# Performance work log

Hardware: AMD Instinct MI355X
Metric: run time of the kernel (lower is better)

Reference implementation:

```python
import jax, jax.numpy as jnp
import numpy as np

T, N, E, F, H, LH = 24, 50000, 1_600_000, 16, 64, 128


def setup_inputs() -> dict:
    key = jax.random.key(0)
    ks = jax.random.split(key, 16)
    s = 0.1  # small init scale
    return {
        "x_seq": jax.random.normal(ks[0], (T, N, F), jnp.float32),
        "edge_index": jax.random.randint(ks[1], (2, E), 0, N, dtype=jnp.int32),
        "W1": jax.random.normal(ks[2], (F, H), jnp.float32) * s,
        "b1": jax.random.normal(ks[3], (H,), jnp.float32) * s,
        "W2": jax.random.normal(ks[4], (H, H), jnp.float32) * s,
        "b2": jax.random.normal(ks[5], (H,), jnp.float32) * s,
        "W_ih": jax.random.normal(ks[6], (4 * LH, H), jnp.float32) * s,
        "W_hh": jax.random.normal(ks[7], (4 * LH, LH), jnp.float32) * s,
        "b_ih": jax.random.normal(ks[8], (4 * LH,), jnp.float32) * s,
        "b_hh": jax.random.normal(ks[9], (4 * LH,), jnp.float32) * s,
        "Wf1": jax.random.normal(ks[10], (LH, 32), jnp.float32) * s,
        "bf1": jax.random.normal(ks[11], (32,), jnp.float32) * s,
        "Wf2": jax.random.normal(ks[12], (32, 1), jnp.float32) * s,
        "bf2": jax.random.normal(ks[13], (1,), jnp.float32) * s,
    }


def reference(x_seq, edge_index, W1, b1, W2, b2, W_ih, W_hh, b_ih, b_hh, Wf1, bf1, Wf2, bf2):
    Nn = x_seq.shape[1]
    lh = W_hh.shape[1]
    src, dst = edge_index[0], edge_index[1]

    # GCN symmetric norm with self-loops: deg counts incoming edges + self-loop
    deg = jax.ops.segment_sum(jnp.ones(src.shape[0], x_seq.dtype), dst, num_segments=Nn) + 1.0
    dinv = jax.lax.rsqrt(deg)
    enorm = dinv[src] * dinv[dst]          # (E,)
    snorm = dinv * dinv                    # (N,) self-loop norm

    def agg(xw):  # xw: (N, H')  -> D^-1/2 (A+I) D^-1/2 xw
        out = jax.ops.segment_sum(xw[src] * enorm[:, None], dst, num_segments=Nn)
        return out + xw * snorm[:, None]

    def gcn_step(_, x_t):  # x_t: (N, F)
        h = jax.nn.relu(agg(x_t @ W1) + b1)
        h = jax.nn.relu(agg(h @ W2) + b2)
        return None, h

    _, h_seq = jax.lax.scan(gcn_step, None, x_seq)  # (T, N, H)

    # single-layer LSTM (torch gate order i, f, g, o); only final h needed
    def lstm_step(carry, x_t):
        h, c = carry
        g = x_t @ W_ih.T + b_ih + h @ W_hh.T + b_hh
        i, f, gg, o = jnp.split(g, 4, axis=-1)
        c = jax.nn.sigmoid(f) * c + jax.nn.sigmoid(i) * jnp.tanh(gg)
        h = jax.nn.sigmoid(o) * jnp.tanh(c)
        return (h, c), None

    h0 = jnp.zeros((Nn, lh), x_seq.dtype)
    (hT, _), _ = jax.lax.scan(lstm_step, (h0, h0), h_seq)

    z = jax.nn.relu(hT @ Wf1 + bf1)
    return (z @ Wf2 + bf2)[:, 0]  # (N,)
```

## Files before the change

### kernel.cpp

```cpp
#include <hip/hip_runtime.h>
#include <hip/hip_bf16.h>
#include <math.h>


typedef short s16x8 __attribute__((ext_vector_type(8)));
typedef float f32x16 __attribute__((ext_vector_type(16)));
typedef unsigned long long u64;
union AF { s16x8 v; u64 q[2]; };

__device__ __forceinline__ float sigf(float x) { return 1.f / (1.f + __expf(-x)); }
__device__ __forceinline__ float tanhfast(float x) { return 1.f - 2.f / (1.f + __expf(2.f * x)); }

__device__ __forceinline__ unsigned bfr(float x) {
    union { float f; unsigned u; } c; c.f = x;
    return (c.u + 0x7fffu + ((c.u >> 16) & 1u)) >> 16;
}
__device__ __forceinline__ void bsplit(float x, unsigned short& hi, unsigned short& lo) {
    unsigned h = bfr(x);
    union { unsigned u; float f; } hf; hf.u = h << 16;
    hi = (unsigned short)h;
    lo = (unsigned short)bfr(x - hf.f);
}
__device__ __forceinline__ float bf2f(unsigned short b) {
    union { unsigned u; float f; } c; c.u = ((unsigned)b) << 16;
    return c.f;
}

__global__ void k_count(const int* __restrict__ dst, int E, int* __restrict__ deg) {
    int e = blockIdx.x * blockDim.x + threadIdx.x;
    if (e < E) atomicAdd(&deg[dst[e]], 1);
}

__global__ void k_dinv(const int* __restrict__ deg, float* __restrict__ dinv, int N) {
    int v = blockIdx.x * blockDim.x + threadIdx.x;
    if (v < N) dinv[v] = rsqrtf((float)deg[v] + 1.0f);
}

__global__ __launch_bounds__(256) void k_scan_part(const int* __restrict__ deg, int* __restrict__ partial, int N) {
    int tid = threadIdx.x;
    int i = blockIdx.x * 256 + tid;
    int v = (i < N) ? deg[i] : 0;
    int s = v;
#pragma unroll
    for (int off = 1; off < 64; off <<= 1) s += __shfl_xor(s, off, 64);
    __shared__ int ws[4];
    if ((tid & 63) == 0) ws[tid >> 6] = s;
    __syncthreads();
    if (tid == 0) partial[blockIdx.x] = ws[0] + ws[1] + ws[2] + ws[3];
}

__global__ __launch_bounds__(256) void k_scan_top(int* __restrict__ partial, int nb) {
    __shared__ int sm[256];
    int t = threadIdx.x;
    int x = (t < nb) ? partial[t] : 0;
    sm[t] = x;
    __syncthreads();
#pragma unroll
    for (int off = 1; off < 256; off <<= 1) {
        int y = (t >= off) ? sm[t - off] : 0;
        __syncthreads();
        sm[t] += y;
        __syncthreads();
    }
    if (t < nb) partial[t] = sm[t] - x;
}

__global__ __launch_bounds__(256) void k_scan_fill(const int* __restrict__ deg, const int* __restrict__ partial,
                                                   int* __restrict__ row_ptr, int* __restrict__ cursor, int N) {
    int tid = threadIdx.x;
    int lane = tid & 63;
    int wv = tid >> 6;
    int i = blockIdx.x * 256 + tid;
    int v = (i < N) ? deg[i] : 0;
    int incl = v;
#pragma unroll
    for (int off = 1; off < 64; off <<= 1) {
        int y = __shfl_up(incl, off, 64);
        if (lane >= off) incl += y;
    }
    __shared__ int ws[4];
    if (lane == 63) ws[wv] = incl;
    __syncthreads();
    int woff = 0;
    for (int w = 0; w < wv; ++w) woff += ws[w];
    int excl = incl - v + woff + partial[blockIdx.x];
    if (i < N) {
        row_ptr[i] = excl;
        cursor[i] = excl;
        if (i == N - 1) row_ptr[N] = excl + v;
    }
}

__global__ void k_fill_range(const int* __restrict__ src, const int* __restrict__ dst, int E,
                             int* __restrict__ cursor, int* __restrict__ col, int lo, int hi) {
    int e = blockIdx.x * blockDim.x + threadIdx.x;
    if (e < E) {
        int d = dst[e];
        if (d >= lo && d < hi) {
            int p = atomicAdd(&cursor[d], 1);
            col[p] = src[e];
        }
    }
}

__global__ void k_wprep(const float* __restrict__ W_ih, const float* __restrict__ W_hh,
                        unsigned short* __restrict__ whi, unsigned short* __restrict__ wlo) {
    int i = blockIdx.x * 256 + threadIdx.x;
    if (i >= 512 * 192) return;
    int g = i / 192, k = i - g * 192;
    float wv = (k < 64) ? W_ih[g * 64 + k] : W_hh[g * 128 + (k - 64)];
    unsigned short h, l;
    bsplit(wv, h, l);
    whi[i] = h;
    wlo[i] = l;
}

__global__ void k_w2prep(const float* __restrict__ W2,
                         unsigned short* __restrict__ w2thi, unsigned short* __restrict__ w2tlo) {
    int i = blockIdx.x * 256 + threadIdx.x;
    if (i >= 64 * 64) return;
    int c = i >> 6, k = i & 63;
    unsigned short h, l;
    bsplit(W2[k * 64 + c], h, l);
    w2thi[c * 64 + k] = h;
    w2tlo[c * 64 + k] = l;
}

__global__ __launch_bounds__(256) void k_gcn1(const float* __restrict__ x, const float* __restrict__ dinv,
                                              const int* __restrict__ row_ptr, const int* __restrict__ col,
                                              const float* __restrict__ W1, const float* __restrict__ b1,
                                              unsigned short* __restrict__ h1bf, int N) {
    __shared__ float w[16 * 64];
    __shared__ float uu[4][16];
    int tid = threadIdx.x;
    ((float4*)w)[tid] = ((const float4*)W1)[tid];
    __syncthreads();
    int lane = tid & 63;
    int wv = tid >> 6;
    int v = blockIdx.x * 4 + wv;
    if (v >= N) return;
    int cg = lane & 7;
    int eg = lane >> 3;
    int b = row_ptr[v];
    int e = row_ptr[v + 1];
    float s0 = 0.f, s1 = 0.f;
#pragma unroll 2
    for (int i = b + eg; i < e; i += 8) {
        int c = col[i];
        float2 xv = *(const float2*)(x + (size_t)c * 16 + 2 * cg);
        float dc = dinv[c];
        s0 = fmaf(dc, xv.x, s0);
        s1 = fmaf(dc, xv.y, s1);
    }
    s0 += __shfl_xor(s0, 8, 64);  s1 += __shfl_xor(s1, 8, 64);
    s0 += __shfl_xor(s0, 16, 64); s1 += __shfl_xor(s1, 16, 64);
    s0 += __shfl_xor(s0, 32, 64); s1 += __shfl_xor(s1, 32, 64);
    float dv = dinv[v];
    if (eg == 0) {
        float2 xv = *(const float2*)(x + (size_t)v * 16 + 2 * cg);
        uu[wv][2 * cg]     = dv * fmaf(dv, xv.x, s0);
        uu[wv][2 * cg + 1] = dv * fmaf(dv, xv.y, s1);
    }
    float a = b1[lane];
#pragma unroll
    for (int k = 0; k < 16; ++k)
        a = fmaf(uu[wv][k], w[k * 64 + lane], a);
    float r1 = fmaxf(a, 0.f) * dv;
    h1bf[(size_t)v * 64 + lane] = (unsigned short)bfr(r1);
}

__global__ __launch_bounds__(256) void k_agg64p(const unsigned short* __restrict__ h1bf,
                                                const float* __restrict__ dinv,
                                                const int* __restrict__ row_ptr, const int* __restrict__ col,
                                                unsigned* __restrict__ vpack, int N) {
    int lane = threadIdx.x & 63;
    int v = blockIdx.x * 4 + (threadIdx.x >> 6);
    if (v >= N) return;
    int cp = lane & 15;
    int eg = lane >> 4;
    int b = row_ptr[v];
    int e = row_ptr[v + 1];
    float s0 = 0.f, s1 = 0.f, s2 = 0.f, s3 = 0.f;
    const uint2* tbl = (const uint2*)h1bf;
#pragma unroll 2
    for (int i = b + eg; i < e; i += 4) {
        int c = col[i];
        uint2 pw = tbl[(size_t)c * 16 + cp];
        s0 += bf2f((unsigned short)(pw.x & 0xffffu));
        s1 += bf2f((unsigned short)(pw.x >> 16));
        s2 += bf2f((unsigned short)(pw.y & 0xffffu));
        s3 += bf2f((unsigned short)(pw.y >> 16));
    }
    s0 += __shfl_xor(s0, 16, 64); s1 += __shfl_xor(s1, 16, 64);
    s2 += __shfl_xor(s2, 16, 64); s3 += __shfl_xor(s3, 16, 64);
    s0 += __shfl_xor(s0, 32, 64); s1 += __shfl_xor(s1, 32, 64);
    s2 += __shfl_xor(s2, 32, 64); s3 += __shfl_xor(s3, 32, 64);
    if (eg == 0) {
        uint2 sw = tbl[(size_t)v * 16 + cp];
        float dv = dinv[v];
        float t0 = dv * (s0 + bf2f((unsigned short)(sw.x & 0xffffu)));
        float t1 = dv * (s1 + bf2f((unsigned short)(sw.x >> 16)));
        float t2 = dv * (s2 + bf2f((unsigned short)(sw.y & 0xffffu)));
        float t3 = dv * (s3 + bf2f((unsigned short)(sw.y >> 16)));
        unsigned short h0, l0, h1v, l1v, h2v, l2v, h3, l3;
        bsplit(t0, h0, l0); bsplit(t1, h1v, l1v);
        bsplit(t2, h2v, l2v); bsplit(t3, h3, l3);
        uint4 o;
        o.x = (unsigned)h0 | ((unsigned)l0 << 16);
        o.y = (unsigned)h1v | ((unsigned)l1v << 16);
        o.z = (unsigned)h2v | ((unsigned)l2v << 16);
        o.w = (unsigned)h3 | ((unsigned)l3 << 16);
        ((uint4*)(vpack + (size_t)v * 64))[cp] = o;
    }
}

__global__ __launch_bounds__(256, 2) void k_h2lstm(const unsigned* __restrict__ vpack,
                                                   const unsigned short* __restrict__ w2thi,
                                                   const unsigned short* __restrict__ w2tlo,
                                                   const float* __restrict__ b2,
                                                   unsigned* __restrict__ hbuf, float* __restrict__ cbuf,
                                                   const unsigned short* __restrict__ whi,
                                                   const unsigned short* __restrict__ wlo,
                                                   const float* __restrict__ b_ih, const float* __restrict__ b_hh,
                                                   int N) {
    __shared__ __align__(16) char lds_hi[64 * 392];
    __shared__ __align__(16) char lds_lo[64 * 392];
    int tid = threadIdx.x;
    int lane = tid & 63;
    int w = tid >> 6;
    int row0 = blockIdx.x * 64;
    int l31 = lane & 31;
    int hf = lane >> 5;

    for (int idx = tid; idx < 64 * 16; idx += 256) {
        int m = idx >> 4;
        int c4 = (idx & 15) * 4;
        int row = row0 + m;
        uint4 pv = make_uint4(0, 0, 0, 0);
        if (row < N) pv = *(const uint4*)(vpack + (size_t)row * 64 + c4);
        u64 hq = (u64)(pv.x & 0xffffu) | ((u64)(pv.y & 0xffffu) << 16) |
                 ((u64)(pv.z & 0xffffu) << 32) | ((u64)(pv.w & 0xffffu) << 48);
        u64 lq = (u64)(pv.x >> 16) | ((u64)(pv.y >> 16) << 16) |
                 ((u64)(pv.z >> 16) << 32) | ((u64)(pv.w >> 16) << 48);
        size_t bo = (size_t)m * 392 + 256 + (size_t)c4 * 2;
        *(u64*)(lds_hi + bo) = hq;
        *(u64*)(lds_lo + bo) = lq;
    }
    for (int idx = tid; idx < 64 * 16; idx += 256) {
        int m = idx >> 4;
        int c4 = (idx & 15) * 4;
        int row = row0 + m;
        uint4 pv = make_uint4(0, 0, 0, 0);
        if (row < N) pv = *(const uint4*)(hbuf + (size_t)row * 128 + c4);
        u64 hq = (u64)(pv.x & 0xffffu) | ((u64)(pv.y & 0xffffu) << 16) |
                 ((u64)(pv.z & 0xffffu) << 32) | ((u64)(pv.w & 0xffffu) << 48);
        u64 lq = (u64)(pv.x >> 16) | ((u64)(pv.y >> 16) << 16) |
                 ((u64)(pv.z >> 16) << 32) | ((u64)(pv.w >> 16) << 48);
        size_t bo = (size_t)m * 392 + 128 + (size_t)c4 * 2;
        *(u64*)(lds_hi + bo) = hq;
        *(u64*)(lds_lo + bo) = lq;
    }
    __syncthreads();

    {
        int rowsub = w & 1, colsub = w >> 1;
        int c = colsub * 32 + l31;
        f32x16 acc;
#pragma unroll
        for (int r = 0; r < 16; ++r) acc[r] = 0.f;
        const char* ah = lds_hi + (size_t)(rowsub * 32 + l31) * 392 + 256 + (size_t)hf * 16;
        const char* al = lds_lo + (size_t)(rowsub * 32 + l31) * 392 + 256 + (size_t)hf * 16;
        const char* bh = (const char*)w2thi + (size_t)c * 128 + (size_t)hf * 16;
        const char* bl = (const char*)w2tlo + (size_t)c * 128 + (size_t)hf * 16;
#pragma unroll
        for (int kc = 0; kc < 4; ++kc) {
            AF Ahi, Alo, Bhi, Blo;
            Ahi.q[0] = *(const u64*)(ah + kc * 32); Ahi.q[1] = *(const u64*)(ah + kc * 32 + 8);
            Alo.q[0] = *(const u64*)(al + kc * 32); Alo.q[1] = *(const u64*)(al + kc * 32 + 8);
            Bhi.v = *(const s16x8*)(bh + kc * 32);
            Blo.v = *(const s16x8*)(bl + kc * 32);
            acc = __builtin_amdgcn_mfma_f32_32x32x16_bf16(Ahi.v, Bhi.v, acc, 0, 0, 0);
            acc = __builtin_amdgcn_mfma_f32_32x32x16_bf16(Alo.v, Bhi.v, acc, 0, 0, 0);
            acc = __builtin_amdgcn_mfma_f32_32x32x16_bf16(Ahi.v, Blo.v, acc, 0, 0, 0);
        }
        float bv = b2[c];
#pragma unroll
        for (int r = 0; r < 16; ++r) {
            int rl = (r & 3) + 8 * (r >> 2) + 4 * hf;
            int m = rowsub * 32 + rl;
            float val = fmaxf(acc[r] + bv, 0.f);
            unsigned short hh, ll;
            bsplit(val, hh, ll);
            size_t bo = (size_t)m * 392 + (size_t)c * 2;
            *(unsigned short*)(lds_hi + bo) = hh;
            *(unsigned short*)(lds_lo + bo) = ll;
        }
    }
    __syncthreads();

    for (int idx = tid; idx < 64 * 16; idx += 256) {
        int m = idx >> 4;
        int c4 = (idx & 15) * 4 + 64;
        int row = row0 + m;
        uint4 pv = make_uint4(0, 0, 0, 0);
        if (row < N) pv = *(const uint4*)(hbuf + (size_t)row * 128 + c4);
        u64 hq = (u64)(pv.x & 0xffffu) | ((u64)(pv.y & 0xffffu) << 16) |
                 ((u64)(pv.z & 0xffffu) << 32) | ((u64)(pv.w & 0xffffu) << 48);
        u64 lq = (u64)(pv.x >> 16) | ((u64)(pv.y >> 16) << 16) |
                 ((u64)(pv.z >> 16) << 32) | ((u64)(pv.w >> 16) << 48);
        size_t bo = (size_t)m * 392 + 256 + (size_t)(c4 - 64) * 2;
        *(u64*)(lds_hi + bo) = hq;
        *(u64*)(lds_lo + bo) = lq;
    }
    __syncthreads();

    int col_j = w * 32 + l31;
    f32x16 acc[2][4];
#pragma unroll
    for (int s = 0; s < 2; ++s)
#pragma unroll
        for (int g = 0; g < 4; ++g)
#pragma unroll
            for (int r = 0; r < 16; ++r) acc[s][g][r] = 0.f;

    const char* whc = (const char*)whi;
    const char* wlc = (const char*)wlo;
    size_t bbase[4];
#pragma unroll
    for (int g = 0; g < 4; ++g) bbase[g] = (size_t)(g * 128 + col_j) * 384 + (size_t)hf * 16;
    size_t abase0 = (size_t)l31 * 392 + (size_t)hf * 16;
    size_t abase1 = (size_t)(32 + l31) * 392 + (size_t)hf * 16;

#pragma unroll
    for (int kc = 0; kc < 12; ++kc) {
        AF ahi0, alo0, ahi1, alo1;
        size_t a0 = abase0 + (size_t)kc * 32;
        size_t a1 = abase1 + (size_t)kc * 32;
        ahi0.q[0] = *(const u64*)(lds_hi + a0); ahi0.q[1] = *(const u64*)(lds_hi + a0 + 8);
        alo0.q[0] = *(const u64*)(lds_lo + a0); alo0.q[1] = *(const u64*)(lds_lo + a0 + 8);
        ahi1.q[0] = *(const u64*)(lds_hi + a1); ahi1.q[1] = *(const u64*)(lds_hi + a1 + 8);
        alo1.q[0] = *(const u64*)(lds_lo + a1); alo1.q[1] = *(const u64*)(lds_lo + a1 + 8);
        AF bhi[4], blo[4];
#pragma unroll
        for (int g = 0; g < 4; ++g) {
            size_t bo = bbase[g] + (size_t)kc * 32;
            bhi[g].v = *(const s16x8*)(whc + bo);
            blo[g].v = *(const s16x8*)(wlc + bo);
        }
#pragma unroll
        for (int g = 0; g < 4; ++g) {
            acc[0][g] = __builtin_amdgcn_mfma_f32_32x32x16_bf16(ahi0.v, bhi[g].v, acc[0][g], 0, 0, 0);
            acc[0][g] = __builtin_amdgcn_mfma_f32_32x32x16_bf16(alo0.v, bhi[g].v, acc[0][g], 0, 0, 0);
            acc[0][g] = __builtin_amdgcn_mfma_f32_32x32x16_bf16(ahi0.v, blo[g].v, acc[0][g], 0, 0, 0);
            acc[1][g] = __builtin_amdgcn_mfma_f32_32x32x16_bf16(ahi1.v, bhi[g].v, acc[1][g], 0, 0, 0);
            acc[1][g] = __builtin_amdgcn_mfma_f32_32x32x16_bf16(alo1.v, bhi[g].v, acc[1][g], 0, 0, 0);
            acc[1][g] = __builtin_amdgcn_mfma_f32_32x32x16_bf16(ahi1.v, blo[g].v, acc[1][g], 0, 0, 0);
        }
    }

    float bi = b_ih[col_j] + b_hh[col_j];
    float bff = b_ih[128 + col_j] + b_hh[128 + col_j];
    float bg = b_ih[256 + col_j] + b_hh[256 + col_j];
    float bo = b_ih[384 + col_j] + b_hh[384 + col_j];
#pragma unroll
    for (int s = 0; s < 2; ++s) {
#pragma unroll
        for (int r = 0; r < 16; ++r) {
            int rl = (r & 3) + 8 * (r >> 2) + 4 * hf;
            int row = row0 + s * 32 + rl;
            if (row < N) {
                size_t off = (size_t)row * 128 + col_j;
                float iv = sigf(acc[s][0][r] + bi);
                float fv = sigf(acc[s][1][r] + bff);
                float gv = tanhfast(acc[s][2][r] + bg);
                float ov = sigf(acc[s][3][r] + bo);
                float cnew = fmaf(fv, cbuf[off], iv * gv);
                float hnew = ov * tanhfast(cnew);
                cbuf[off] = cnew;
                unsigned short hh, hl;
                bsplit(hnew, hh, hl);
                hbuf[off] = (unsigned)hh | ((unsigned)hl << 16);
            }
        }
    }
}

__global__ __launch_bounds__(256) void k_mlp(const unsigned* __restrict__ hbuf, const float* __restrict__ Wf1,
                                             const float* __restrict__ bf1, const float* __restrict__ Wf2,
                                             const float* __restrict__ bf2, float* __restrict__ out, int N) {
    int lane = threadIdx.x & 63;
    int v = blockIdx.x * 4 + (threadIdx.x >> 6);
    if (v >= N) return;
    int j = lane & 31;
    int half = lane >> 5;
    const unsigned* hr = hbuf + (size_t)v * 128 + half * 64;
    float s = 0.f;
#pragma unroll
    for (int k = 0; k < 64; ++k) {
        unsigned pw = hr[k];
        float hv = bf2f((unsigned short)(pw & 0xffffu)) + bf2f((unsigned short)(pw >> 16));
        s = fmaf(hv, Wf1[(half * 64 + k) * 32 + j], s);
    }
    s += __shfl_down(s, 32, 64);
    float z = fmaxf(s + bf1[j], 0.f);
    float p = z * Wf2[j];
#pragma unroll
    for (int off = 16; off > 0; off >>= 1) p += __shfl_down(p, off, 64);
    if (lane == 0) out[v] = p + bf2[0];
}

extern "C" void kernel_launch(void* const* d_in, const int* in_sizes, int n_in,
                              void* d_out, int out_size, void* d_ws, size_t ws_size,
                              hipStream_t stream) {
    const float* x_seq = (const float*)d_in[0];
    const int* eidx = (const int*)d_in[1];
    const float* W1 = (const float*)d_in[2];
    const float* b1 = (const float*)d_in[3];
    const float* W2 = (const float*)d_in[4];
    const float* b2 = (const float*)d_in[5];
    const float* W_ih = (const float*)d_in[6];
    const float* W_hh = (const float*)d_in[7];
    const float* b_ih = (const float*)d_in[8];
    const float* b_hh = (const float*)d_in[9];
    const float* Wf1 = (const float*)d_in[10];
    const float* bf1 = (const float*)d_in[11];
    const float* Wf2 = (const float*)d_in[12];
    const float* bf2 = (const float*)d_in[13];

    int N = out_size;
    int E = in_sizes[1] / 2;
    int T = in_sizes[0] / (N * 16);
    const int* srcp = eidx;
    const int* dstp = eidx + E;

    char* ws = (char*)d_ws;
    size_t off = 0;
    auto alloc = [&](size_t bytes) -> char* {
        char* p = ws + off;
        off = (off + bytes + 255) & ~(size_t)255;
        return p;
    };
    int* deg = (int*)alloc((size_t)N * 4);
    int* row_ptr = (int*)alloc(((size_t)N + 1) * 4);
    int* cursor = (int*)alloc((size_t)N * 4);
    int* col = (int*)alloc((size_t)E * 4);
    int* partial = (int*)alloc(260 * 4);
    float* dinv = (float*)alloc((size_t)N * 4);
    unsigned short* h1bf = (unsigned short*)alloc((size_t)N * 64 * 2);
    unsigned* vpack = (unsigned*)alloc((size_t)N * 64 * 4);
    unsigned* hbuf = (unsigned*)alloc((size_t)N * 128 * 4);
    float* cbuf = (float*)alloc((size_t)N * 128 * 4);
    unsigned short* whi = (unsigned short*)alloc((size_t)512 * 192 * 2);
    unsigned short* wlo = (unsigned short*)alloc((size_t)512 * 192 * 2);
    unsigned short* w2thi = (unsigned short*)alloc((size_t)64 * 64 * 2);
    unsigned short* w2tlo = (unsigned short*)alloc((size_t)64 * 64 * 2);

    hipMemsetAsync(deg, 0, (size_t)N * 4, stream);
    hipMemsetAsync(hbuf, 0, (size_t)N * 128 * 4, stream);
    hipMemsetAsync(cbuf, 0, (size_t)N * 128 * 4, stream);

    int nb = (N + 255) / 256;
    k_count<<<(E + 255) / 256, 256, 0, stream>>>(dstp, E, deg);
    k_dinv<<<(N + 255) / 256, 256, 0, stream>>>(deg, dinv, N);
    k_scan_part<<<nb, 256, 0, stream>>>(deg, partial, N);
    k_scan_top<<<1, 256, 0, stream>>>(partial, nb);
    k_scan_fill<<<nb, 256, 0, stream>>>(deg, partial, row_ptr, cursor, N);
    int halfN = N / 2;
    k_fill_range<<<(E + 255) / 256, 256, 0, stream>>>(srcp, dstp, E, cursor, col, 0, halfN);
    k_fill_range<<<(E + 255) / 256, 256, 0, stream>>>(srcp, dstp, E, cursor, col, halfN, N);
    k_wprep<<<(512 * 192 + 255) / 256, 256, 0, stream>>>(W_ih, W_hh, whi, wlo);
    k_w2prep<<<(64 * 64 + 255) / 256, 256, 0, stream>>>(W2, w2thi, w2tlo);

    int node_wave_blocks = (N + 3) / 4;
    int tile_blocks = (N + 63) / 64;
    for (int t = 0; t < T; ++t) {
        const float* xt = x_seq + (size_t)t * N * 16;
        k_gcn1<<<node_wave_blocks, 256, 0, stream>>>(xt, dinv, row_ptr, col, W1, b1, h1bf, N);
        k_agg64p<<<node_wave_blocks, 256, 0, stream>>>(h1bf, dinv, row_ptr, col, vpack, N);
        k_h2lstm<<<tile_blocks, 256, 0, stream>>>(vpack, w2thi, w2tlo, b2, hbuf, cbuf,
                                                  whi, wlo, b_ih, b_hh, N);
    }
    k_mlp<<<node_wave_blocks, 256, 0, stream>>>(hbuf, Wf1, bf1, Wf2, bf2, (float*)d_out, N);
}
```

Before: 4.112 ms.

## Split interleaved hi/lo bf16 buffers into planar arrays and cut LSTM register pressure

The interleaved hi|lo packed 32-bit buffers for the aggregated features and LSTM hidden state become separate planar bf16 hi and lo arrays. This lets the LSTM kernel copy them straight into LDS with 16-byte loads instead of unpacking and repacking bits. The LSTM GEMM now processes the two 32-row subtiles one after another with a single accumulator set instead of holding both at once, and launch bounds go from 2 to 3 blocks per SM. The aim is less load/ALU overhead and higher occupancy, at the cost of the B-weight fragments being reloaded for each subtile.

```diff
diff --git a/kernel.cpp b/kernel.cpp
--- a/kernel.cpp
+++ b/kernel.cpp
@@ -6,7 +6,8 @@
 typedef short s16x8 __attribute__((ext_vector_type(8)));
 typedef float f32x16 __attribute__((ext_vector_type(16)));
 typedef unsigned long long u64;
-union AF { s16x8 v; u64 q[2]; };
+typedef unsigned short u16;
+union AF { s16x8 v; u64 q[2]; uint4 u4; };
 
 __device__ __forceinline__ float sigf(float x) { return 1.f / (1.f + __expf(-x)); }
 __device__ __forceinline__ float tanhfast(float x) { return 1.f - 2.f / (1.f + __expf(2.f * x)); }
@@ -15,13 +16,13 @@
     union { float f; unsigned u; } c; c.f = x;
     return (c.u + 0x7fffu + ((c.u >> 16) & 1u)) >> 16;
 }
-__device__ __forceinline__ void bsplit(float x, unsigned short& hi, unsigned short& lo) {
+__device__ __forceinline__ void bsplit(float x, u16& hi, u16& lo) {
     unsigned h = bfr(x);
     union { unsigned u; float f; } hf; hf.u = h << 16;
-    hi = (unsigned short)h;
-    lo = (unsigned short)bfr(x - hf.f);
-}
-__device__ __forceinline__ float bf2f(unsigned short b) {
+    hi = (u16)h;
+    lo = (u16)bfr(x - hf.f);
+}
+__device__ __forceinline__ float bf2f(u16 b) {
     union { unsigned u; float f; } c; c.u = ((unsigned)b) << 16;
     return c.f;
 }
@@ -104,23 +105,23 @@
 }
 
 __global__ void k_wprep(const float* __restrict__ W_ih, const float* __restrict__ W_hh,
-                        unsigned short* __restrict__ whi, unsigned short* __restrict__ wlo) {
+                        u16* __restrict__ whi, u16* __restrict__ wlo) {
     int i = blockIdx.x * 256 + threadIdx.x;
     if (i >= 512 * 192) return;
     int g = i / 192, k = i - g * 192;
     float wv = (k < 64) ? W_ih[g * 64 + k] : W_hh[g * 128 + (k - 64)];
-    unsigned short h, l;
+    u16 h, l;
     bsplit(wv, h, l);
     whi[i] = h;
     wlo[i] = l;
 }
 
 __global__ void k_w2prep(const float* __restrict__ W2,
-                         unsigned short* __restrict__ w2thi, unsigned short* __restrict__ w2tlo) {
+                         u16* __restrict__ w2thi, u16* __restrict__ w2tlo) {
     int i = blockIdx.x * 256 + threadIdx.x;
     if (i >= 64 * 64) return;
     int c = i >> 6, k = i & 63;
-    unsigned short h, l;
+    u16 h, l;
     bsplit(W2[k * 64 + c], h, l);
     w2thi[c * 64 + k] = h;
     w2tlo[c * 64 + k] = l;
@@ -129,7 +130,7 @@
 __global__ __launch_bounds__(256) void k_gcn1(const float* __restrict__ x, const float* __restrict__ dinv,
                                               const int* __restrict__ row_ptr, const int* __restrict__ col,
                                               const float* __restrict__ W1, const float* __restrict__ b1,
-                                              unsigned short* __restrict__ h1bf, int N) {
+                                              u16* __restrict__ h1bf, int N) {
     __shared__ float w[16 * 64];
     __shared__ float uu[4][16];
     int tid = threadIdx.x;
@@ -166,13 +167,13 @@
     for (int k = 0; k < 16; ++k)
         a = fmaf(uu[wv][k], w[k * 64 + lane], a);
     float r1 = fmaxf(a, 0.f) * dv;
-    h1bf[(size_t)v * 64 + lane] = (unsigned short)bfr(r1);
-}
-
-__global__ __launch_bounds__(256) void k_agg64p(const unsigned short* __restrict__ h1bf,
+    h1bf[(size_t)v * 64 + lane] = (u16)bfr(r1);
+}
+
+__global__ __launch_bounds__(256) void k_agg64p(const u16* __restrict__ h1bf,
                                                 const float* __restrict__ dinv,
                                                 const int* __restrict__ row_ptr, const int* __restrict__ col,
-                                                unsigned* __restrict__ vpack, int N) {
+                                                u16* __restrict__ vhi, u16* __restrict__ vlo, int N) {
     int lane = threadIdx.x & 63;
     int v = blockIdx.x * 4 + (threadIdx.x >> 6);
     if (v >= N) return;
@@ -186,10 +187,10 @@
     for (int i = b + eg; i < e; i += 4) {
         int c = col[i];
         uint2 pw = tbl[(size_t)c * 16 + cp];
-        s0 += bf2f((unsigned short)(pw.x & 0xffffu));
-        s1 += bf2f((unsigned short)(pw.x >> 16));
-        s2 += bf2f((unsigned short)(pw.y & 0xffffu));
-        s3 += bf2f((unsigned short)(pw.y >> 16));
+        s0 += bf2f((u16)(pw.x & 0xffffu));
+        s1 += bf2f((u16)(pw.x >> 16));
+        s2 += bf2f((u16)(pw.y & 0xffffu));
+        s3 += bf2f((u16)(pw.y >> 16));
     }
     s0 += __shfl_xor(s0, 16, 64); s1 += __shfl_xor(s1, 16, 64);
     s2 += __shfl_xor(s2, 16, 64); s3 += __shfl_xor(s3, 16, 64);
@@ -198,29 +199,29 @@
     if (eg == 0) {
         uint2 sw = tbl[(size_t)v * 16 + cp];
         float dv = dinv[v];
-        float t0 = dv * (s0 + bf2f((unsigned short)(sw.x & 0xffffu)));
-        float t1 = dv * (s1 + bf2f((unsigned short)(sw.x >> 16)));
-        float t2 = dv * (s2 + bf2f((unsigned short)(sw.y & 0xffffu)));
-        float t3 = dv * (s3 + bf2f((unsigned short)(sw.y >> 16)));
-        unsigned short h0, l0, h1v, l1v, h2v, l2v, h3, l3;
+        float t0 = dv * (s0 + bf2f((u16)(sw.x & 0xffffu)));
+        float t1 = dv * (s1 + bf2f((u16)(sw.x >> 16)));
+        float t2 = dv * (s2 + bf2f((u16)(sw.y & 0xffffu)));
+        float t3 = dv * (s3 + bf2f((u16)(sw.y >> 16)));
+        u16 h0, l0, h1v, l1v, h2v, l2v, h3, l3;
         bsplit(t0, h0, l0); bsplit(t1, h1v, l1v);
         bsplit(t2, h2v, l2v); bsplit(t3, h3, l3);
-        uint4 o;
-        o.x = (unsigned)h0 | ((unsigned)l0 << 16);
-        o.y = (unsigned)h1v | ((unsigned)l1v << 16);
-        o.z = (unsigned)h2v | ((unsigned)l2v << 16);
-        o.w = (unsigned)h3 | ((unsigned)l3 << 16);
-        ((uint4*)(vpack + (size_t)v * 64))[cp] = o;
-    }
-}
-
-__global__ __launch_bounds__(256, 2) void k_h2lstm(const unsigned* __restrict__ vpack,
-                                                   const unsigned short* __restrict__ w2thi,
-                                                   const unsigned short* __restrict__ w2tlo,
+        uint2 oh, ol;
+        oh.x = (unsigned)h0 | ((unsigned)h1v << 16);
+        oh.y = (unsigned)h2v | ((unsigned)h3 << 16);
+        ol.x = (unsigned)l0 | ((unsigned)l1v << 16);
+        ol.y = (unsigned)l2v | ((unsigned)l3 << 16);
+        *(uint2*)(vhi + (size_t)v * 64 + 4 * cp) = oh;
+        *(uint2*)(vlo + (size_t)v * 64 + 4 * cp) = ol;
+    }
+}
+
+__global__ __launch_bounds__(256, 3) void k_h2lstm(const u16* __restrict__ vhi, const u16* __restrict__ vlo,
+                                                   const u16* __restrict__ w2thi, const u16* __restrict__ w2tlo,
                                                    const float* __restrict__ b2,
-                                                   unsigned* __restrict__ hbuf, float* __restrict__ cbuf,
-                                                   const unsigned short* __restrict__ whi,
-                                                   const unsigned short* __restrict__ wlo,
+                                                   u16* __restrict__ hhi, u16* __restrict__ hlo,
+                                                   float* __restrict__ cbuf,
+                                                   const u16* __restrict__ whi, const u16* __restrict__ wlo,
                                                    const float* __restrict__ b_ih, const float* __restrict__ b_hh,
                                                    int N) {
     __shared__ __align__(16) char lds_hi[64 * 392];
@@ -232,33 +233,29 @@
     int l31 = lane & 31;
     int hf = lane >> 5;
 
-    for (int idx = tid; idx < 64 * 16; idx += 256) {
-        int m = idx >> 4;
-        int c4 = (idx & 15) * 4;
+    for (int idx = tid; idx < 512; idx += 256) {
+        int m = idx >> 3, c8 = idx & 7;
         int row = row0 + m;
-        uint4 pv = make_uint4(0, 0, 0, 0);
-        if (row < N) pv = *(const uint4*)(vpack + (size_t)row * 64 + c4);
-        u64 hq = (u64)(pv.x & 0xffffu) | ((u64)(pv.y & 0xffffu) << 16) |
-                 ((u64)(pv.z & 0xffffu) << 32) | ((u64)(pv.w & 0xffffu) << 48);
-        u64 lq = (u64)(pv.x >> 16) | ((u64)(pv.y >> 16) << 16) |
-                 ((u64)(pv.z >> 16) << 32) | ((u64)(pv.w >> 16) << 48);
-        size_t bo = (size_t)m * 392 + 256 + (size_t)c4 * 2;
-        *(u64*)(lds_hi + bo) = hq;
-        *(u64*)(lds_lo + bo) = lq;
-    }
-    for (int idx = tid; idx < 64 * 16; idx += 256) {
-        int m = idx >> 4;
-        int c4 = (idx & 15) * 4;
+        uint4 vh = make_uint4(0, 0, 0, 0), vl = make_uint4(0, 0, 0, 0);
+        if (row < N) {
+            vh = *(const uint4*)(vhi + (size_t)row * 64 + c8 * 8);
+            vl = *(const uint4*)(vlo + (size_t)row * 64 + c8 * 8);
+        }
+        size_t bo = (size_t)m * 392 + 256 + (size_t)c8 * 16;
+        *(uint4*)(lds_hi + bo) = vh;
+        *(uint4*)(lds_lo + bo) = vl;
+    }
+    for (int idx = tid; idx < 512; idx += 256) {
+        int m = idx >> 3, c8 = idx & 7;
         int row = row0 + m;
-        uint4 pv = make_uint4(0, 0, 0, 0);
-        if (row < N) pv = *(const uint4*)(hbuf + (size_t)row * 128 + c4);
-        u64 hq = (u64)(pv.x & 0xffffu) | ((u64)(pv.y & 0xffffu) << 16) |
-                 ((u64)(pv.z & 0xffffu) << 32) | ((u64)(pv.w & 0xffffu) << 48);
-        u64 lq = (u64)(pv.x >> 16) | ((u64)(pv.y >> 16) << 16) |
-                 ((u64)(pv.z >> 16) << 32) | ((u64)(pv.w >> 16) << 48);
-        size_t bo = (size_t)m * 392 + 128 + (size_t)c4 * 2;
-        *(u64*)(lds_hi + bo) = hq;
-        *(u64*)(lds_lo + bo) = lq;
+        uint4 vh = make_uint4(0, 0, 0, 0), vl = make_uint4(0, 0, 0, 0);
+        if (row < N) {
+            vh = *(const uint4*)(hhi + (size_t)row * 128 + c8 * 8);
+            vl = *(const uint4*)(hlo + (size_t)row * 128 + c8 * 8);
+        }
+        size_t bo = (size_t)m * 392 + 128 + (size_t)c8 * 16;
+        *(uint4*)(lds_hi + bo) = vh;
+        *(uint4*)(lds_lo + bo) = vl;
     }
     __syncthreads();
 
@@ -289,116 +286,104 @@
             int rl = (r & 3) + 8 * (r >> 2) + 4 * hf;
             int m = rowsub * 32 + rl;
             float val = fmaxf(acc[r] + bv, 0.f);
-            unsigned short hh, ll;
+            u16 hh, ll;
             bsplit(val, hh, ll);
             size_t bo = (size_t)m * 392 + (size_t)c * 2;
-            *(unsigned short*)(lds_hi + bo) = hh;
-            *(unsigned short*)(lds_lo + bo) = ll;
-        }
-    }
-    __syncthreads();
-
-    for (int idx = tid; idx < 64 * 16; idx += 256) {
-        int m = idx >> 4;
-        int c4 = (idx & 15) * 4 + 64;
+            *(u16*)(lds_hi + bo) = hh;
+            *(u16*)(lds_lo + bo) = ll;
+        }
+    }
+    __syncthreads();
+
+    for (int idx = tid; idx < 512; idx += 256) {
+        int m = idx >> 3, c8 = idx & 7;
         int row = row0 + m;
-        uint4 pv = make_uint4(0, 0, 0, 0);
-        if (row < N) pv = *(const uint4*)(hbuf + (size_t)row * 128 + c4);
-        u64 hq = (u64)(pv.x & 0xffffu) | ((u64)(pv.y & 0xffffu) << 16) |
-                 ((u64)(pv.z & 0xffffu) << 32) | ((u64)(pv.w & 0xffffu) << 48);
-        u64 lq = (u64)(pv.x >> 16) | ((u64)(pv.y >> 16) << 16) |
-                 ((u64)(pv.z >> 16) << 32) | ((u64)(pv.w >> 16) << 48);
-        size_t bo = (size_t)m * 392 + 256 + (size_t)(c4 - 64) * 2;
-        *(u64*)(lds_hi + bo) = hq;
-        *(u64*)(lds_lo + bo) = lq;
+        uint4 vh = make_uint4(0, 0, 0, 0), vl = make_uint4(0, 0, 0, 0);
+        if (row < N) {
+            vh = *(const uint4*)(hhi + (size_t)row * 128 + 64 + c8 * 8);
+            vl = *(const uint4*)(hlo + (size_t)row * 128 + 64 + c8 * 8);
+        }
+        size_t bo = (size_t)m * 392 + 256 + (size_t)c8 * 16;
+        *(uint4*)(lds_hi + bo) = vh;
+        *(uint4*)(lds_lo + bo) = vl;
     }
     __syncthreads();
 
     int col_j = w * 32 + l31;
-    f32x16 acc[2][4];
-#pragma unroll
-    for (int s = 0; s < 2; ++s)
-#pragma unroll
-        for (int g = 0; g < 4; ++g)
-#pragma unroll
-            for (int r = 0; r < 16; ++r) acc[s][g][r] = 0.f;
-
     const char* whc = (const char*)whi;
     const char* wlc = (const char*)wlo;
     size_t bbase[4];
 #pragma unroll
     for (int g = 0; g < 4; ++g) bbase[g] = (size_t)(g * 128 + col_j) * 384 + (size_t)hf * 16;
-    size_t abase0 = (size_t)l31 * 392 + (size_t)hf * 16;
-    size_t abase1 = (size_t)(32 + l31) * 392 + (size_t)hf * 16;
-
-#pragma unroll
-    for (int kc = 0; kc < 12; ++kc) {
-        AF ahi0, alo0, ahi1, alo1;
-        size_t a0 = abase0 + (size_t)kc * 32;
-        size_t a1 = abase1 + (size_t)kc * 32;
-        ahi0.q[0] = *(const u64*)(lds_hi + a0); ahi0.q[1] = *(const u64*)(lds_hi + a0 + 8);
-        alo0.q[0] = *(const u64*)(lds_lo + a0); alo0.q[1] = *(const u64*)(lds_lo + a0 + 8);
-        ahi1.q[0] = *(const u64*)(lds_hi + a1); ahi1.q[1] = *(const u64*)(lds_hi + a1 + 8);
-        alo1.q[0] = *(const u64*)(lds_lo + a1); alo1.q[1] = *(const u64*)(lds_lo + a1 + 8);
-        AF bhi[4], blo[4];
-#pragma unroll
-        for (int g = 0; g < 4; ++g) {
-            size_t bo = bbase[g] + (size_t)kc * 32;
-            bhi[g].v = *(const s16x8*)(whc + bo);
-            blo[g].v = *(const s16x8*)(wlc + bo);
-        }
-#pragma unroll
-        for (int g = 0; g < 4; ++g) {
-            acc[0][g] = __builtin_amdgcn_mfma_f32_32x32x16_bf16(ahi0.v, bhi[g].v, acc[0][g], 0, 0, 0);
-            acc[0][g] = __builtin_amdgcn_mfma_f32_32x32x16_bf16(alo0.v, bhi[g].v, acc[0][g], 0, 0, 0);
-            acc[0][g] = __builtin_amdgcn_mfma_f32_32x32x16_bf16(ahi0.v, blo[g].v, acc[0][g], 0, 0, 0);
-            acc[1][g] = __builtin_amdgcn_mfma_f32_32x32x16_bf16(ahi1.v, bhi[g].v, acc[1][g], 0, 0, 0);
-            acc[1][g] = __builtin_amdgcn_mfma_f32_32x32x16_bf16(alo1.v, bhi[g].v, acc[1][g], 0, 0, 0);
-            acc[1][g] = __builtin_amdgcn_mfma_f32_32x32x16_bf16(ahi1.v, blo[g].v, acc[1][g], 0, 0, 0);
-        }
-    }
-
     float bi = b_ih[col_j] + b_hh[col_j];
     float bff = b_ih[128 + col_j] + b_hh[128 + col_j];
     float bg = b_ih[256 + col_j] + b_hh[256 + col_j];
     float bo = b_ih[384 + col_j] + b_hh[384 + col_j];
-#pragma unroll
+
     for (int s = 0; s < 2; ++s) {
+        f32x16 acc[4];
+#pragma unroll
+        for (int g = 0; g < 4; ++g)
+#pragma unroll
+            for (int r = 0; r < 16; ++r) acc[g][r] = 0.f;
+        size_t abase = (size_t)(s * 32 + l31) * 392 + (size_t)hf * 16;
+#pragma unroll
+        for (int kc = 0; kc < 12; ++kc) {
+            AF ahi, alo;
+            size_t a0 = abase + (size_t)kc * 32;
+            ahi.q[0] = *(const u64*)(lds_hi + a0); ahi.q[1] = *(const u64*)(lds_hi + a0 + 8);
+            alo.q[0] = *(const u64*)(lds_lo + a0); alo.q[1] = *(const u64*)(lds_lo + a0 + 8);
+            AF bhi[4], blo[4];
+#pragma unroll
+            for (int g = 0; g < 4; ++g) {
+                size_t bo2 = bbase[g] + (size_t)kc * 32;
+                bhi[g].v = *(const s16x8*)(whc + bo2);
+                blo[g].v = *(const s16x8*)(wlc + bo2);
+            }
+#pragma unroll
+            for (int g = 0; g < 4; ++g) {
+                acc[g] = __builtin_amdgcn_mfma_f32_32x32x16_bf16(ahi.v, bhi[g].v, acc[g], 0, 0, 0);
+                acc[g] = __builtin_amdgcn_mfma_f32_32x32x16_bf16(alo.v, bhi[g].v, acc[g], 0, 0, 0);
+                acc[g] = __builtin_amdgcn_mfma_f32_32x32x16_bf16(ahi.v, blo[g].v, acc[g], 0, 0, 0);
+            }
+        }
 #pragma unroll
         for (int r = 0; r < 16; ++r) {
             int rl = (r & 3) + 8 * (r >> 2) + 4 * hf;
             int row = row0 + s * 32 + rl;
             if (row < N) {
                 size_t off = (size_t)row * 128 + col_j;
-                float iv = sigf(acc[s][0][r] + bi);
-                float fv = sigf(acc[s][1][r] + bff);
-                float gv = tanhfast(acc[s][2][r] + bg);
-                float ov = sigf(acc[s][3][r] + bo);
+                float iv = sigf(acc[0][r] + bi);
+                float fv = sigf(acc[1][r] + bff);
+                float gv = tanhfast(acc[2][r] + bg);
+                float ov = sigf(acc[3][r] + bo);
                 float cnew = fmaf(fv, cbuf[off], iv * gv);
                 float hnew = ov * tanhfast(cnew);
                 cbuf[off] = cnew;
-                unsigned short hh, hl;
+                u16 hh, hl;
                 bsplit(hnew, hh, hl);
-                hbuf[off] = (unsigned)hh | ((unsigned)hl << 16);
+                hhi[off] = hh;
+                hlo[off] = hl;
             }
         }
     }
 }
 
-__global__ __launch_bounds__(256) void k_mlp(const unsigned* __restrict__ hbuf, const float* __restrict__ Wf1,
-                                             const float* __restrict__ bf1, const float* __restrict__ Wf2,
-                                             const float* __restrict__ bf2, float* __restrict__ out, int N) {
+__global__ __launch_bounds__(256) void k_mlp(const u16* __restrict__ hhi, const u16* __restrict__ hlo,
+                                             const float* __restrict__ Wf1, const float* __restrict__ bf1,
+                                             const float* __restrict__ Wf2, const float* __restrict__ bf2,
+                                             float* __restrict__ out, int N) {
     int lane = threadIdx.x & 63;
     int v = blockIdx.x * 4 + (threadIdx.x >> 6);
     if (v >= N) return;
     int j = lane & 31;
     int half = lane >> 5;
-    const unsigned* hr = hbuf + (size_t)v * 128 + half * 64;
+    const u16* hh = hhi + (size_t)v * 128 + half * 64;
+    const u16* hl = hlo + (size_t)v * 128 + half * 64;
     float s = 0.f;
 #pragma unroll
     for (int k = 0; k < 64; ++k) {
-        unsigned pw = hr[k];
-        float hv = bf2f((unsigned short)(pw & 0xffffu)) + bf2f((unsigned short)(pw >> 16));
+        float hv = bf2f(hh[k]) + bf2f(hl[k]);
         s = fmaf(hv, Wf1[(half * 64 + k) * 32 + j], s);
     }
     s += __shfl_down(s, 32, 64);
@@ -446,17 +431,20 @@
     int* col = (int*)alloc((size_t)E * 4);
     int* partial = (int*)alloc(260 * 4);
     float* dinv = (float*)alloc((size_t)N * 4);
-    unsigned short* h1bf = (unsigned short*)alloc((size_t)N * 64 * 2);
-    unsigned* vpack = (unsigned*)alloc((size_t)N * 64 * 4);
-    unsigned* hbuf = (unsigned*)alloc((size_t)N * 128 * 4);
+    u16* h1bf = (u16*)alloc((size_t)N * 64 * 2);
+    u16* vhi = (u16*)alloc((size_t)N * 64 * 2);
+    u16* vlo = (u16*)alloc((size_t)N * 64 * 2);
+    u16* hhi = (u16*)alloc((size_t)N * 128 * 2);
+    u16* hlo = (u16*)alloc((size_t)N * 128 * 2);
     float* cbuf = (float*)alloc((size_t)N * 128 * 4);
-    unsigned short* whi = (unsigned short*)alloc((size_t)512 * 192 * 2);
-    unsigned short* wlo = (unsigned short*)alloc((size_t)512 * 192 * 2);
-    unsigned short* w2thi = (unsigned short*)alloc((size_t)64 * 64 * 2);
-    unsigned short* w2tlo = (unsigned short*)alloc((size_t)64 * 64 * 2);
+    u16* whi = (u16*)alloc((size_t)512 * 192 * 2);
+    u16* wlo = (u16*)alloc((size_t)512 * 192 * 2);
+    u16* w2thi = (u16*)alloc((size_t)64 * 64 * 2);
+    u16* w2tlo = (u16*)alloc((size_t)64 * 64 * 2);
 
     hipMemsetAsync(deg, 0, (size_t)N * 4, stream);
-    hipMemsetAsync(hbuf, 0, (size_t)N * 128 * 4, stream);
+    hipMemsetAsync(hhi, 0, (size_t)N * 128 * 2, stream);
+    hipMemsetAsync(hlo, 0, (size_t)N * 128 * 2, stream);
     hipMemsetAsync(cbuf, 0, (size_t)N * 128 * 4, stream);
 
     int nb = (N + 255) / 256;
@@ -476,9 +464,9 @@
     for (int t = 0; t < T; ++t) {
         const float* xt = x_seq + (size_t)t * N * 16;
         k_gcn1<<<node_wave_blocks, 256, 0, stream>>>(xt, dinv, row_ptr, col, W1, b1, h1bf, N);
-        k_agg64p<<<node_wave_blocks, 256, 0, stream>>>(h1bf, dinv, row_ptr, col, vpack, N);
-        k_h2lstm<<<tile_blocks, 256, 0, stream>>>(vpack, w2thi, w2tlo, b2, hbuf, cbuf,
+        k_agg64p<<<node_wave_blocks, 256, 0, stream>>>(h1bf, dinv, row_ptr, col, vhi, vlo, N);
+        k_h2lstm<<<tile_blocks, 256, 0, stream>>>(vhi, vlo, w2thi, w2tlo, b2, hhi, hlo, cbuf,
                                                   whi, wlo, b_ih, b_hh, N);
     }
-    k_mlp<<<node_wave_blocks, 256, 0, stream>>>(hbuf, Wf1, bf1, Wf2, bf2, (float*)d_out, N);
-}
+    k_mlp<<<node_wave_blocks, 256, 0, stream>>>(hhi, hlo, Wf1, bf1, Wf2, bf2, (float*)d_out, N);
+}
```

Measured after the change: 8.437 ms. 105% more time.
